# Kernel optimization log

Measured on AMD Instinct MI355X. Metric: run time of the kernel, lower is better.

Reference implementation:

```python
import jax, jax.numpy as jnp
import numpy as np


def setup_inputs() -> dict:
    key = jax.random.key(0)
    ks = jax.random.split(key, 8)
    B, S, H, E = 4, 4096, 768, 64
    hidden_states = jax.random.normal(ks[0], (B, S, H), dtype=jnp.float32)
    attention_mask = jnp.ones((B, S), dtype=jnp.float32)
    entity_positions = jax.random.randint(ks[1], (B, E), 0, S)
    scale = 1.0 / np.sqrt(H)
    Wq = jax.random.normal(ks[2], (H, H), dtype=jnp.float32) * scale
    bq = jnp.zeros((H,), dtype=jnp.float32)
    Wk = jax.random.normal(ks[3], (H, H), dtype=jnp.float32) * scale
    bk = jnp.zeros((H,), dtype=jnp.float32)
    Wv = jax.random.normal(ks[4], (H, H), dtype=jnp.float32) * scale
    bv = jnp.zeros((H,), dtype=jnp.float32)
    return {"hidden_states": hidden_states, "attention_mask": attention_mask,
            "entity_positions": entity_positions,
            "Wq": Wq, "bq": bq, "Wk": Wk, "bk": bk, "Wv": Wv, "bv": bv}


def reference(hidden_states, attention_mask, entity_positions, Wq, bq, Wk, bk, Wv, bv):
    B, S, H = hidden_states.shape
    scaling = jnp.sqrt(jnp.asarray(H, dtype=jnp.float32))
    # Linear layers (torch: x @ W.T + b)
    q = jnp.einsum('bsh,oh->bso', hidden_states, Wq) + bq
    k = jnp.einsum('bsh,oh->bso', hidden_states, Wk) + bk
    v = jnp.einsum('bsh,oh->bso', hidden_states, Wv) + bv
    scores = jnp.einsum('bqh,bkh->bqk', q, k) / scaling  # [B,S,S]
    # Entity bias: +1.0 added to every row at each entity column (duplicates accumulate).
    # Equivalent to a per-key-column bias broadcast over query rows.
    bias_cols = jnp.zeros((B, S), dtype=scores.dtype)
    batch_idx = jnp.arange(B)[:, None]  # [B,1] broadcast against [B,E]
    bias_cols = bias_cols.at[batch_idx, entity_positions].add(1.0)
    scores = scores + bias_cols[:, None, :]
    # Attention mask over key columns.
    scores = scores + (1.0 - attention_mask)[:, None, :] * -10000.0
    probs = jax.nn.softmax(scores, axis=-1)
    context = jnp.einsum('bqk,bkh->bqh', probs, v)
    return context
```

## Files before the change

### kernel.cpp

```cpp
#include <hip/hip_runtime.h>


typedef short bf16x8 __attribute__((ext_vector_type(8)));
typedef float f32x4 __attribute__((ext_vector_type(4)));
typedef float f32x16 __attribute__((ext_vector_type(16)));

#define MFMA16(a, b, c) __builtin_amdgcn_mfma_f32_16x16x32_bf16(a, b, c, 0, 0, 0)
#define MFMA32(a, b, c) __builtin_amdgcn_mfma_f32_32x32x16_bf16(a, b, c, 0, 0, 0)

#define ASM_BAR() asm volatile("s_barrier" ::: "memory")
#define ASM_WAITV0() asm volatile("s_waitcnt vmcnt(0)" ::: "memory")
#define ASM_WAITV4() asm volatile("s_waitcnt vmcnt(4)" ::: "memory")
#define ASM_WAITV6() asm volatile("s_waitcnt vmcnt(6)" ::: "memory")
#define ASM_WAITL0() asm volatile("s_waitcnt lgkmcnt(0)" ::: "memory")

__device__ __forceinline__ unsigned short f2bf(float f) {
  unsigned u = __float_as_uint(f);
  u = u + 0x7FFFu + ((u >> 16) & 1u);
  return (unsigned short)(u >> 16);
}

__device__ __forceinline__ void gll16(const void* g, void* l) {
  __builtin_amdgcn_global_load_lds(
      (const __attribute__((address_space(1))) unsigned int*)g,
      (__attribute__((address_space(3))) unsigned int*)l, 16, 0, 0);
}

#define SCALE_L2E 0.05205877316f
#define LOG2E 1.4426950408889634f

__global__ void convert_w_kernel(const float* __restrict__ w0, const float* __restrict__ w1,
                                 const float* __restrict__ w2, unsigned short* __restrict__ o0,
                                 unsigned short* __restrict__ o1, unsigned short* __restrict__ o2) {
  const int which = blockIdx.y;
  const float* s = which == 0 ? w0 : (which == 1 ? w1 : w2);
  unsigned short* d = which == 0 ? o0 : (which == 1 ? o1 : o2);
  const int i = (blockIdx.x * 256 + threadIdx.x) * 4;
  float4 v = *(const float4*)(s + i);
  ushort4 r = make_ushort4(f2bf(v.x), f2bf(v.y), f2bf(v.z), f2bf(v.w));
  *(ushort4*)(d + i) = r;
}

__global__ void convert_hs_kernel(const float* __restrict__ hs, unsigned short* __restrict__ o) {
  const int i = (blockIdx.x * 256 + threadIdx.x) * 4;
  float4 v = *(const float4*)(hs + i);
  ushort4 r = make_ushort4(f2bf(v.x), f2bf(v.y), f2bf(v.z), f2bf(v.w));
  *(ushort4*)(o + i) = r;
}

__global__ void kb_init_kernel(const float* __restrict__ mask, float* __restrict__ kb) {
  const int i = blockIdx.x * 256 + threadIdx.x;
  kb[i] = (1.0f - mask[i]) * (-10000.0f * LOG2E);
}

__global__ void kb_scatter_kernel(const int* __restrict__ ep, float* __restrict__ kb) {
  const int t = threadIdx.x;
  const int b = t >> 6, e = t & 63;
  const int pos = ep[b * 64 + e];
  atomicAdd(kb + b * 4096 + pos, LOG2E);
}

__global__ __launch_bounds__(256, 3) void gemm_qk_kernel(
    const unsigned short* __restrict__ hsb, const unsigned short* __restrict__ Wqb,
    const unsigned short* __restrict__ Wkb, const float* __restrict__ bq,
    const float* __restrict__ bk, unsigned short* __restrict__ Qb,
    unsigned short* __restrict__ Kb) {
  const int z = blockIdx.z;
  const unsigned short* W = z ? Wkb : Wqb;
  const float* bias = z ? bk : bq;
  unsigned short* out = z ? Kb : Qb;
  const int m0 = blockIdx.x * 128;
  const int n0 = blockIdx.y * 128;

  __shared__ __align__(16) unsigned short Ab[3][128 * 32];
  __shared__ __align__(16) unsigned short Bb[3][128 * 32];

  const int t = threadIdx.x;
  const int lane = t & 63;
  const int w = t >> 6;
  const int wm = w & 1, wn = w >> 1;

  f32x4 acc[4][4] = {};

  auto issueT = [&](const unsigned short* src, int base, int kk, unsigned short* dst) {
#pragma unroll
    for (int r = 0; r < 2; r++) {
      int u = r * 256 + t;
      int o = u >> 2, cc = u & 3;
      int c = cc ^ ((o >> 1) & 3);
      gll16(src + (size_t)(base + o) * 768 + kk + c * 8, dst + u * 8);
    }
  };

  issueT(hsb, m0, 0, Ab[0]);
  issueT(W, n0, 0, Bb[0]);
  issueT(hsb, m0, 32, Ab[1]);
  issueT(W, n0, 32, Bb[1]);
  ASM_WAITV4();
  ASM_BAR();

  for (int k = 0; k < 24; k++) {
    const int buf = k % 3;
    if (k < 22) {
      const int nb = (k + 2) % 3;
      issueT(hsb, m0, (k + 2) * 32, Ab[nb]);
      issueT(W, n0, (k + 2) * 32, Bb[nb]);
    }
    bf16x8 af[4], bfr[4];
#pragma unroll
    for (int mt = 0; mt < 4; mt++) {
      int row = wm * 64 + mt * 16 + (lane & 15);
      int cc = (lane >> 4) ^ ((row >> 1) & 3);
      af[mt] = *(const bf16x8*)(&Ab[buf][row * 32 + cc * 8]);
    }
#pragma unroll
    for (int nt = 0; nt < 4; nt++) {
      int row = wn * 64 + nt * 16 + (lane & 15);
      int cc = (lane >> 4) ^ ((row >> 1) & 3);
      bfr[nt] = *(const bf16x8*)(&Bb[buf][row * 32 + cc * 8]);
    }
#pragma unroll
    for (int mt = 0; mt < 4; mt++)
#pragma unroll
      for (int nt = 0; nt < 4; nt++) acc[mt][nt] = MFMA16(af[mt], bfr[nt], acc[mt][nt]);
    if (k < 22) {
      ASM_WAITV4();
    } else {
      ASM_WAITV0();
    }
    ASM_BAR();
  }

#pragma unroll
  for (int nt = 0; nt < 4; nt++) {
    int col = n0 + wn * 64 + nt * 16 + (lane & 15);
    float bv = bias[col];
#pragma unroll
    for (int mt = 0; mt < 4; mt++) {
#pragma unroll
      for (int i = 0; i < 4; i++) {
        int row = m0 + wm * 64 + mt * 16 + (lane >> 4) * 4 + i;
        out[(size_t)row * 768 + col] = f2bf(acc[mt][nt][i] + bv);
      }
    }
  }
}

__global__ __launch_bounds__(256, 3) void gemm_vt_kernel(const unsigned short* __restrict__ hsb,
                                                         const unsigned short* __restrict__ Wvb,
                                                         const float* __restrict__ bv,
                                                         unsigned short* __restrict__ Vt) {
  const int m0 = blockIdx.x * 128;
  const int n0 = blockIdx.y * 128;

  __shared__ __align__(16) unsigned short Ab[3][128 * 32];
  __shared__ __align__(16) unsigned short Bb[3][128 * 32];

  const int t = threadIdx.x;
  const int lane = t & 63;
  const int w = t >> 6;
  const int wm = w & 1, wn = w >> 1;

  f32x4 acc[4][4] = {};

  auto issueT = [&](const unsigned short* src, int base, int kk, unsigned short* dst) {
#pragma unroll
    for (int r = 0; r < 2; r++) {
      int u = r * 256 + t;
      int o = u >> 2, cc = u & 3;
      int c = cc ^ ((o >> 1) & 3);
      gll16(src + (size_t)(base + o) * 768 + kk + c * 8, dst + u * 8);
    }
  };

  issueT(Wvb, m0, 0, Ab[0]);
  issueT(hsb, n0, 0, Bb[0]);
  issueT(Wvb, m0, 32, Ab[1]);
  issueT(hsb, n0, 32, Bb[1]);
  ASM_WAITV4();
  ASM_BAR();

  for (int k = 0; k < 24; k++) {
    const int buf = k % 3;
    if (k < 22) {
      const int nb = (k + 2) % 3;
      issueT(Wvb, m0, (k + 2) * 32, Ab[nb]);
      issueT(hsb, n0, (k + 2) * 32, Bb[nb]);
    }
    bf16x8 af[4], bfr[4];
#pragma unroll
    for (int mt = 0; mt < 4; mt++) {
      int row = wm * 64 + mt * 16 + (lane & 15);
      int cc = (lane >> 4) ^ ((row >> 1) & 3);
      af[mt] = *(const bf16x8*)(&Ab[buf][row * 32 + cc * 8]);
    }
#pragma unroll
    for (int nt = 0; nt < 4; nt++) {
      int row = wn * 64 + nt * 16 + (lane & 15);
      int cc = (lane >> 4) ^ ((row >> 1) & 3);
      bfr[nt] = *(const bf16x8*)(&Bb[buf][row * 32 + cc * 8]);
    }
#pragma unroll
    for (int mt = 0; mt < 4; mt++)
#pragma unroll
      for (int nt = 0; nt < 4; nt++) acc[mt][nt] = MFMA16(af[mt], bfr[nt], acc[mt][nt]);
    if (k < 22) {
      ASM_WAITV4();
    } else {
      ASM_WAITV0();
    }
    ASM_BAR();
  }

#pragma unroll
  for (int mt = 0; mt < 4; mt++) {
#pragma unroll
    for (int i = 0; i < 4; i++) {
      int row_o = m0 + wm * 64 + mt * 16 + (lane >> 4) * 4 + i;
      float bb = bv[row_o];
#pragma unroll
      for (int nt = 0; nt < 4; nt++) {
        int mcol = n0 + wn * 64 + nt * 16 + (lane & 15);
        int bat = mcol >> 12, s = mcol & 4095;
        Vt[(size_t)bat * 768 * 4096 + (size_t)row_o * 4096 + s] = f2bf(acc[mt][nt][i] + bb);
      }
    }
  }
}

__global__ __launch_bounds__(512, 2) void flash_kernel(const unsigned short* __restrict__ Qb,
                                                       const unsigned short* __restrict__ Kb,
                                                       const unsigned short* __restrict__ Vt,
                                                       const float* __restrict__ KB,
                                                       float* __restrict__ out) {
  __shared__ __align__(16) unsigned short kbuf[32 * 768];
  __shared__ __align__(16) unsigned short vbuf[768 * 32];
  __shared__ __align__(16) unsigned short pbuf[4 * 64 * 8];
  __shared__ __align__(16) float sx[4 * 2 * 64 * 16];
  __shared__ __align__(16) float kb_lds[4096];
  __shared__ float st_l[64];

  const int t = threadIdx.x;
  const int lane = t & 63;
  const int w = t >> 6;
  const int rg = w & 1, hg = w >> 1;
  const int mt2 = w & 1, dg = w >> 1;
  const int flat = blockIdx.x;
  const int b = flat & 3, qt = flat >> 2;
  const int q0 = qt * 64;

  const unsigned short* Qg = Qb + (size_t)b * 4096 * 768;
  const unsigned short* Kg = Kb + (size_t)b * 4096 * 768;
  const unsigned short* Vg = Vt + (size_t)b * 768 * 4096;
  const float* KBb = KB + b * 4096;

  bf16x8 qf[12];
  {
    const unsigned short* qp =
        Qg + (size_t)(q0 + rg * 32 + (lane & 31)) * 768 + hg * 192 + (lane >> 5) * 8;
#pragma unroll
    for (int c = 0; c < 12; c++) qf[c] = *(const bf16x8*)(qp + c * 16);
  }
#pragma unroll
  for (int r = 0; r < 2; r++) {
    int i = t * 8 + r * 4;
    *(float4*)(kb_lds + i) = *(const float4*)(KBb + i);
  }

  int kidx[12];
  {
    const int key = lane & 31, l5 = lane >> 5, sw = (key >> 1) & 3;
#pragma unroll
    for (int c = 0; c < 12; c++) {
      int g = hg * 24 + c * 2 + l5;
      kidx[c] = ((g >> 2) * 128 + key * 4 + ((g & 3) ^ sw)) * 8;
    }
  }
  int vbase;
  {
    int d0 = dg * 192 + (lane & 15);
    vbase = (d0 * 4 + ((lane >> 4) ^ ((d0 >> 1) & 3))) * 8;
  }
  int pidx0, pidx1;
  {
    int g2 = lane >> 4;
    int r0 = mt2 * 32 + (lane & 15);
    pidx0 = (g2 * 64 + (r0 ^ (g2 * 2))) * 8;
    pidx1 = (g2 * 64 + ((r0 + 16) ^ (g2 * 2))) * 8;
  }
  const int s_rg = t >> 8, s_q = (t >> 6) & 3, s_l = t & 63;
  const int col = s_l & 31;
  const int row_b = s_rg * 32 + 8 * s_q + 4 * (s_l >> 5);
  int pslot[4];
#pragma unroll
  for (int jj = 0; jj < 4; jj++)
    pslot[jj] = ((col >> 3) * 64 + ((row_b + jj) ^ ((col >> 3) * 2))) * 8 + (col & 7);
  float* sxw = sx + hg * 2048 + (rg * 64 + lane) * 16;
  const int wswz = (lane >> 1) & 3;
  const float* sxr = sx + (s_rg * 64 + s_l) * 16 + (s_q ^ ((s_l >> 1) & 3)) * 4;

  f32x4 oacc[24] = {};
  float racc0 = 0.0f, racc1 = 0.0f, racc2 = 0.0f, racc3 = 0.0f;

  auto issueK = [&](int j) {
#pragma unroll
    for (int r = 0; r < 6; r++) {
      int u = r * 512 + t;
      int ks = u >> 7, rem = u & 127, key = rem >> 2, cs = rem & 3;
      int c = cs ^ ((key >> 1) & 3);
      gll16(Kg + (size_t)(j * 32 + key) * 768 + ks * 32 + c * 8, &kbuf[u * 8]);
    }
  };
  auto issueV = [&](int j) {
#pragma unroll
    for (int r = 0; r < 6; r++) {
      int u = r * 512 + t;
      int d = u >> 2, cs = u & 3;
      int c = cs ^ ((d >> 1) & 3);
      gll16(Vg + (size_t)d * 4096 + j * 32 + c * 8, &vbuf[u * 8]);
    }
  };

  issueK(0);
  ASM_WAITV0();
  ASM_BAR();

  for (int j = 0; j < 128; j++) {
    issueV(j);
    f32x16 s = {};
#pragma unroll
    for (int c = 0; c < 12; c++) {
      bf16x8 kf = *(const bf16x8*)(kbuf + kidx[c]);
      s = MFMA32(qf[c], kf, s);
    }
#pragma unroll
    for (int i = 0; i < 4; i++) {
      *(float4*)(sxw + (i ^ wswz) * 4) =
          make_float4(s[i * 4], s[i * 4 + 1], s[i * 4 + 2], s[i * 4 + 3]);
    }
    ASM_WAITL0();
    ASM_BAR();
    if (j < 127) issueK(j + 1);
    {
      float4 a0 = *(const float4*)(sxr);
      float4 a1 = *(const float4*)(sxr + 2048);
      float4 a2 = *(const float4*)(sxr + 4096);
      float4 a3 = *(const float4*)(sxr + 6144);
      float kbias = kb_lds[j * 32 + col];
      float e0 = __builtin_amdgcn_exp2f(fmaf(a0.x + a1.x + a2.x + a3.x, SCALE_L2E, kbias));
      float e1 = __builtin_amdgcn_exp2f(fmaf(a0.y + a1.y + a2.y + a3.y, SCALE_L2E, kbias));
      float e2 = __builtin_amdgcn_exp2f(fmaf(a0.z + a1.z + a2.z + a3.z, SCALE_L2E, kbias));
      float e3 = __builtin_amdgcn_exp2f(fmaf(a0.w + a1.w + a2.w + a3.w, SCALE_L2E, kbias));
      pbuf[pslot[0]] = f2bf(e0);
      pbuf[pslot[1]] = f2bf(e1);
      pbuf[pslot[2]] = f2bf(e2);
      pbuf[pslot[3]] = f2bf(e3);
      racc0 += e0;
      racc1 += e1;
      racc2 += e2;
      racc3 += e3;
    }
    ASM_WAITL0();
    if (j < 127) {
      ASM_WAITV6();
    } else {
      ASM_WAITV0();
    }
    ASM_BAR();
    {
      bf16x8 pf0 = *(const bf16x8*)(pbuf + pidx0);
      bf16x8 pf1 = *(const bf16x8*)(pbuf + pidx1);
#pragma unroll
      for (int dt = 0; dt < 12; dt++) {
        bf16x8 vf = *(const bf16x8*)(vbuf + vbase + dt * 512);
        oacc[dt] = MFMA16(pf0, vf, oacc[dt]);
        oacc[12 + dt] = MFMA16(pf1, vf, oacc[12 + dt]);
      }
    }
    ASM_WAITV0();
    ASM_BAR();
  }
#pragma unroll
  for (int m = 1; m < 32; m <<= 1) {
    racc0 += __shfl_xor(racc0, m, 32);
    racc1 += __shfl_xor(racc1, m, 32);
    racc2 += __shfl_xor(racc2, m, 32);
    racc3 += __shfl_xor(racc3, m, 32);
  }
  if ((s_l & 31) == 0) {
    st_l[row_b] = racc0;
    st_l[row_b + 1] = racc1;
    st_l[row_b + 2] = racc2;
    st_l[row_b + 3] = racc3;
  }
  __syncthreads();
#pragma unroll
  for (int pt = 0; pt < 2; pt++) {
    int rb = mt2 * 32 + pt * 16 + (lane >> 4) * 4;
    float l0 = 1.0f / st_l[rb], l1 = 1.0f / st_l[rb + 1];
    float l2 = 1.0f / st_l[rb + 2], l3 = 1.0f / st_l[rb + 3];
#pragma unroll
    for (int dt = 0; dt < 12; dt++) {
      int d = dg * 192 + dt * 16 + (lane & 15);
      size_t base = ((size_t)(b * 4096 + q0 + rb)) * 768 + d;
      out[base] = oacc[pt * 12 + dt][0] * l0;
      out[base + 768] = oacc[pt * 12 + dt][1] * l1;
      out[base + 2 * 768] = oacc[pt * 12 + dt][2] * l2;
      out[base + 3 * 768] = oacc[pt * 12 + dt][3] * l3;
    }
  }
}

extern "C" void kernel_launch(void* const* d_in, const int* in_sizes, int n_in, void* d_out,
                              int out_size, void* d_ws, size_t ws_size, hipStream_t stream) {
  const float* hs = (const float*)d_in[0];
  const float* mask = (const float*)d_in[1];
  const int* ep = (const int*)d_in[2];
  const float* Wq = (const float*)d_in[3];
  const float* bq = (const float*)d_in[4];
  const float* Wk = (const float*)d_in[5];
  const float* bk = (const float*)d_in[6];
  const float* Wv = (const float*)d_in[7];
  const float* bv = (const float*)d_in[8];
  float* outp = (float*)d_out;

  char* ws = (char*)d_ws;
  unsigned short* Qb = (unsigned short*)(ws);
  unsigned short* Kb = (unsigned short*)(ws + 25165824);
  unsigned short* Vt = (unsigned short*)(ws + 50331648);
  unsigned short* Wqb = (unsigned short*)(ws + 75497472);
  unsigned short* Wkb = (unsigned short*)(ws + 76677120);
  unsigned short* Wvb = (unsigned short*)(ws + 77856768);
  float* KBp = (float*)(ws + 79036416);
  unsigned short* Hsb = (unsigned short*)(ws + 79101952);

  convert_w_kernel<<<dim3(576, 3), 256, 0, stream>>>(Wq, Wk, Wv, Wqb, Wkb, Wvb);
  convert_hs_kernel<<<12288, 256, 0, stream>>>(hs, Hsb);
  kb_init_kernel<<<64, 256, 0, stream>>>(mask, KBp);
  kb_scatter_kernel<<<1, 256, 0, stream>>>(ep, KBp);
  gemm_qk_kernel<<<dim3(128, 6, 2), 256, 0, stream>>>(Hsb, Wqb, Wkb, bq, bk, Qb, Kb);
  gemm_vt_kernel<<<dim3(6, 128), 256, 0, stream>>>(Hsb, Wvb, bv, Vt);
  flash_kernel<<<256, 512, 0, stream>>>(Qb, Kb, Vt, KBp, outp);
}
```

Baseline: 484.0 us.

## Merge prep kernels and QKV GEMMs into single launches, tweak P LDS swizzle

Four small preprocessing kernels (weight/hidden-state bf16 conversion, key-bias init, entity scatter) are folded into one prep kernel, and the entity bias is now computed by per-column counting instead of atomics. The Q/K GEMM and the transposed V GEMM become one launch of 2304 blocks dispatched by block index. The flash kernel's P-buffer swizzle gains an extra XOR bit to reduce LDS bank conflicts. The aim is to cut launch overhead and tail gaps between kernels, at the cost of some branching and extra index arithmetic.

New measurement: 477.7 us, median of 2. No clear change (-1.3%).

```diff
diff --git a/kernel.cpp b/kernel.cpp
--- a/kernel.cpp
+++ b/kernel.cpp
@@ -29,56 +29,77 @@
 #define SCALE_L2E 0.05205877316f
 #define LOG2E 1.4426950408889634f
 
-__global__ void convert_w_kernel(const float* __restrict__ w0, const float* __restrict__ w1,
-                                 const float* __restrict__ w2, unsigned short* __restrict__ o0,
-                                 unsigned short* __restrict__ o1, unsigned short* __restrict__ o2) {
-  const int which = blockIdx.y;
-  const float* s = which == 0 ? w0 : (which == 1 ? w1 : w2);
-  unsigned short* d = which == 0 ? o0 : (which == 1 ? o1 : o2);
-  const int i = (blockIdx.x * 256 + threadIdx.x) * 4;
-  float4 v = *(const float4*)(s + i);
-  ushort4 r = make_ushort4(f2bf(v.x), f2bf(v.y), f2bf(v.z), f2bf(v.w));
-  *(ushort4*)(d + i) = r;
-}
-
-__global__ void convert_hs_kernel(const float* __restrict__ hs, unsigned short* __restrict__ o) {
-  const int i = (blockIdx.x * 256 + threadIdx.x) * 4;
-  float4 v = *(const float4*)(hs + i);
-  ushort4 r = make_ushort4(f2bf(v.x), f2bf(v.y), f2bf(v.z), f2bf(v.w));
-  *(ushort4*)(o + i) = r;
-}
-
-__global__ void kb_init_kernel(const float* __restrict__ mask, float* __restrict__ kb) {
-  const int i = blockIdx.x * 256 + threadIdx.x;
-  kb[i] = (1.0f - mask[i]) * (-10000.0f * LOG2E);
-}
-
-__global__ void kb_scatter_kernel(const int* __restrict__ ep, float* __restrict__ kb) {
+#define HS_BLOCKS 12288
+#define W_BLOCKS 1728
+#define KB_BLOCKS 64
+__global__ void prep_kernel(const float* __restrict__ hs, unsigned short* __restrict__ ohs,
+                            const float* __restrict__ w0, const float* __restrict__ w1,
+                            const float* __restrict__ w2, unsigned short* __restrict__ o0,
+                            unsigned short* __restrict__ o1, unsigned short* __restrict__ o2,
+                            const float* __restrict__ mask, const int* __restrict__ ep,
+                            float* __restrict__ kb) {
+  __shared__ int eps[64];
+  const int bid = blockIdx.x;
   const int t = threadIdx.x;
-  const int b = t >> 6, e = t & 63;
-  const int pos = ep[b * 64 + e];
-  atomicAdd(kb + b * 4096 + pos, LOG2E);
-}
-
-__global__ __launch_bounds__(256, 3) void gemm_qk_kernel(
+  if (bid < HS_BLOCKS) {
+    const int i = (bid * 256 + t) * 4;
+    float4 v = *(const float4*)(hs + i);
+    *(ushort4*)(ohs + i) = make_ushort4(f2bf(v.x), f2bf(v.y), f2bf(v.z), f2bf(v.w));
+  } else if (bid < HS_BLOCKS + W_BLOCKS) {
+    const int wb = bid - HS_BLOCKS;
+    const int which = wb / 576;
+    const float* s = which == 0 ? w0 : (which == 1 ? w1 : w2);
+    unsigned short* d = which == 0 ? o0 : (which == 1 ? o1 : o2);
+    const int i = ((wb - which * 576) * 256 + t) * 4;
+    float4 v = *(const float4*)(s + i);
+    *(ushort4*)(d + i) = make_ushort4(f2bf(v.x), f2bf(v.y), f2bf(v.z), f2bf(v.w));
+  } else {
+    const int s = (bid - HS_BLOCKS - W_BLOCKS) * 256 + t;
+    const int b = s >> 12;
+    if (t < 64) eps[t] = ep[b * 64 + t];
+    __syncthreads();
+    const int sp = s & 4095;
+    float cnt = 0.0f;
+#pragma unroll 8
+    for (int e = 0; e < 64; e++) cnt += (eps[e] == sp) ? 1.0f : 0.0f;
+    kb[s] = (1.0f - mask[s]) * (-10000.0f * LOG2E) + cnt * LOG2E;
+  }
+}
+
+__global__ __launch_bounds__(256, 3) void gemm_qkv_kernel(
     const unsigned short* __restrict__ hsb, const unsigned short* __restrict__ Wqb,
-    const unsigned short* __restrict__ Wkb, const float* __restrict__ bq,
-    const float* __restrict__ bk, unsigned short* __restrict__ Qb,
-    unsigned short* __restrict__ Kb) {
-  const int z = blockIdx.z;
-  const unsigned short* W = z ? Wkb : Wqb;
-  const float* bias = z ? bk : bq;
-  unsigned short* out = z ? Kb : Qb;
-  const int m0 = blockIdx.x * 128;
-  const int n0 = blockIdx.y * 128;
-
+    const unsigned short* __restrict__ Wkb, const unsigned short* __restrict__ Wvb,
+    const float* __restrict__ bq, const float* __restrict__ bk, const float* __restrict__ bv,
+    unsigned short* __restrict__ Qb, unsigned short* __restrict__ Kb,
+    unsigned short* __restrict__ Vt) {
   __shared__ __align__(16) unsigned short Ab[3][128 * 32];
   __shared__ __align__(16) unsigned short Bb[3][128 * 32];
 
+  const int bid = blockIdx.x;
   const int t = threadIdx.x;
   const int lane = t & 63;
   const int w = t >> 6;
   const int wm = w & 1, wn = w >> 1;
+
+  const bool is_vt = bid >= 1536;
+  const unsigned short* srcA;
+  const unsigned short* srcB;
+  int m0, n0, z = 0;
+  if (!is_vt) {
+    z = bid / 768;
+    const int r = bid - z * 768;
+    m0 = (r & 127) * 128;
+    n0 = (r >> 7) * 128;
+    srcA = hsb;
+    srcB = z ? Wkb : Wqb;
+  } else {
+    const int r = bid - 1536;
+    const int mx = r % 6;
+    m0 = mx * 128;
+    n0 = (r / 6) * 128;
+    srcA = Wvb;
+    srcB = hsb;
+  }
 
   f32x4 acc[4][4] = {};
 
@@ -92,10 +113,10 @@
     }
   };
 
-  issueT(hsb, m0, 0, Ab[0]);
-  issueT(W, n0, 0, Bb[0]);
-  issueT(hsb, m0, 32, Ab[1]);
-  issueT(W, n0, 32, Bb[1]);
+  issueT(srcA, m0, 0, Ab[0]);
+  issueT(srcB, n0, 0, Bb[0]);
+  issueT(srcA, m0, 32, Ab[1]);
+  issueT(srcB, n0, 32, Bb[1]);
   ASM_WAITV4();
   ASM_BAR();
 
@@ -103,8 +124,8 @@
     const int buf = k % 3;
     if (k < 22) {
       const int nb = (k + 2) % 3;
-      issueT(hsb, m0, (k + 2) * 32, Ab[nb]);
-      issueT(W, n0, (k + 2) * 32, Bb[nb]);
+      issueT(srcA, m0, (k + 2) * 32, Ab[nb]);
+      issueT(srcB, n0, (k + 2) * 32, Bb[nb]);
     }
     bf16x8 af[4], bfr[4];
 #pragma unroll
@@ -131,98 +152,35 @@
     ASM_BAR();
   }
 
-#pragma unroll
-  for (int nt = 0; nt < 4; nt++) {
-    int col = n0 + wn * 64 + nt * 16 + (lane & 15);
-    float bv = bias[col];
+  if (!is_vt) {
+    const float* bias = z ? bk : bq;
+    unsigned short* out = z ? Kb : Qb;
+#pragma unroll
+    for (int nt = 0; nt < 4; nt++) {
+      int col = n0 + wn * 64 + nt * 16 + (lane & 15);
+      float bv_ = bias[col];
+#pragma unroll
+      for (int mt = 0; mt < 4; mt++) {
+#pragma unroll
+        for (int i = 0; i < 4; i++) {
+          int row = m0 + wm * 64 + mt * 16 + (lane >> 4) * 4 + i;
+          out[(size_t)row * 768 + col] = f2bf(acc[mt][nt][i] + bv_);
+        }
+      }
+    }
+  } else {
 #pragma unroll
     for (int mt = 0; mt < 4; mt++) {
 #pragma unroll
       for (int i = 0; i < 4; i++) {
-        int row = m0 + wm * 64 + mt * 16 + (lane >> 4) * 4 + i;
-        out[(size_t)row * 768 + col] = f2bf(acc[mt][nt][i] + bv);
-      }
-    }
-  }
-}
-
-__global__ __launch_bounds__(256, 3) void gemm_vt_kernel(const unsigned short* __restrict__ hsb,
-                                                         const unsigned short* __restrict__ Wvb,
-                                                         const float* __restrict__ bv,
-                                                         unsigned short* __restrict__ Vt) {
-  const int m0 = blockIdx.x * 128;
-  const int n0 = blockIdx.y * 128;
-
-  __shared__ __align__(16) unsigned short Ab[3][128 * 32];
-  __shared__ __align__(16) unsigned short Bb[3][128 * 32];
-
-  const int t = threadIdx.x;
-  const int lane = t & 63;
-  const int w = t >> 6;
-  const int wm = w & 1, wn = w >> 1;
-
-  f32x4 acc[4][4] = {};
-
-  auto issueT = [&](const unsigned short* src, int base, int kk, unsigned short* dst) {
-#pragma unroll
-    for (int r = 0; r < 2; r++) {
-      int u = r * 256 + t;
-      int o = u >> 2, cc = u & 3;
-      int c = cc ^ ((o >> 1) & 3);
-      gll16(src + (size_t)(base + o) * 768 + kk + c * 8, dst + u * 8);
-    }
-  };
-
-  issueT(Wvb, m0, 0, Ab[0]);
-  issueT(hsb, n0, 0, Bb[0]);
-  issueT(Wvb, m0, 32, Ab[1]);
-  issueT(hsb, n0, 32, Bb[1]);
-  ASM_WAITV4();
-  ASM_BAR();
-
-  for (int k = 0; k < 24; k++) {
-    const int buf = k % 3;
-    if (k < 22) {
-      const int nb = (k + 2) % 3;
-      issueT(Wvb, m0, (k + 2) * 32, Ab[nb]);
-      issueT(hsb, n0, (k + 2) * 32, Bb[nb]);
-    }
-    bf16x8 af[4], bfr[4];
-#pragma unroll
-    for (int mt = 0; mt < 4; mt++) {
-      int row = wm * 64 + mt * 16 + (lane & 15);
-      int cc = (lane >> 4) ^ ((row >> 1) & 3);
-      af[mt] = *(const bf16x8*)(&Ab[buf][row * 32 + cc * 8]);
-    }
-#pragma unroll
-    for (int nt = 0; nt < 4; nt++) {
-      int row = wn * 64 + nt * 16 + (lane & 15);
-      int cc = (lane >> 4) ^ ((row >> 1) & 3);
-      bfr[nt] = *(const bf16x8*)(&Bb[buf][row * 32 + cc * 8]);
-    }
-#pragma unroll
-    for (int mt = 0; mt < 4; mt++)
-#pragma unroll
-      for (int nt = 0; nt < 4; nt++) acc[mt][nt] = MFMA16(af[mt], bfr[nt], acc[mt][nt]);
-    if (k < 22) {
-      ASM_WAITV4();
-    } else {
-      ASM_WAITV0();
-    }
-    ASM_BAR();
-  }
-
-#pragma unroll
-  for (int mt = 0; mt < 4; mt++) {
-#pragma unroll
-    for (int i = 0; i < 4; i++) {
-      int row_o = m0 + wm * 64 + mt * 16 + (lane >> 4) * 4 + i;
-      float bb = bv[row_o];
-#pragma unroll
-      for (int nt = 0; nt < 4; nt++) {
-        int mcol = n0 + wn * 64 + nt * 16 + (lane & 15);
-        int bat = mcol >> 12, s = mcol & 4095;
-        Vt[(size_t)bat * 768 * 4096 + (size_t)row_o * 4096 + s] = f2bf(acc[mt][nt][i] + bb);
+        int row_o = m0 + wm * 64 + mt * 16 + (lane >> 4) * 4 + i;
+        float bb = bv[row_o];
+#pragma unroll
+        for (int nt = 0; nt < 4; nt++) {
+          int mcol = n0 + wn * 64 + nt * 16 + (lane & 15);
+          int bat = mcol >> 12, s = mcol & 4095;
+          Vt[(size_t)bat * 768 * 4096 + (size_t)row_o * 4096 + s] = f2bf(acc[mt][nt][i] + bb);
+        }
       }
     }
   }
@@ -285,16 +243,19 @@
   {
     int g2 = lane >> 4;
     int r0 = mt2 * 32 + (lane & 15);
-    pidx0 = (g2 * 64 + (r0 ^ (g2 * 2))) * 8;
-    pidx1 = (g2 * 64 + ((r0 + 16) ^ (g2 * 2))) * 8;
+    int r1 = r0 + 16;
+    pidx0 = (g2 * 64 + (r0 ^ (g2 * 2) ^ ((r0 >> 2) & 1))) * 8;
+    pidx1 = (g2 * 64 + (r1 ^ (g2 * 2) ^ ((r1 >> 2) & 1))) * 8;
   }
   const int s_rg = t >> 8, s_q = (t >> 6) & 3, s_l = t & 63;
   const int col = s_l & 31;
   const int row_b = s_rg * 32 + 8 * s_q + 4 * (s_l >> 5);
   int pslot[4];
 #pragma unroll
-  for (int jj = 0; jj < 4; jj++)
-    pslot[jj] = ((col >> 3) * 64 + ((row_b + jj) ^ ((col >> 3) * 2))) * 8 + (col & 7);
+  for (int jj = 0; jj < 4; jj++) {
+    int rw = row_b + jj;
+    pslot[jj] = ((col >> 3) * 64 + (rw ^ ((col >> 3) * 2) ^ ((rw >> 2) & 1))) * 8 + (col & 7);
+  }
   float* sxw = sx + hg * 2048 + (rg * 64 + lane) * 16;
   const int wswz = (lane >> 1) & 3;
   const float* sxr = sx + (s_rg * 64 + s_l) * 16 + (s_q ^ ((s_l >> 1) & 3)) * 4;
@@ -434,11 +395,8 @@
   float* KBp = (float*)(ws + 79036416);
   unsigned short* Hsb = (unsigned short*)(ws + 79101952);
 
-  convert_w_kernel<<<dim3(576, 3), 256, 0, stream>>>(Wq, Wk, Wv, Wqb, Wkb, Wvb);
-  convert_hs_kernel<<<12288, 256, 0, stream>>>(hs, Hsb);
-  kb_init_kernel<<<64, 256, 0, stream>>>(mask, KBp);
-  kb_scatter_kernel<<<1, 256, 0, stream>>>(ep, KBp);
-  gemm_qk_kernel<<<dim3(128, 6, 2), 256, 0, stream>>>(Hsb, Wqb, Wkb, bq, bk, Qb, Kb);
-  gemm_vt_kernel<<<dim3(6, 128), 256, 0, stream>>>(Hsb, Wvb, bv, Vt);
+  prep_kernel<<<HS_BLOCKS + W_BLOCKS + KB_BLOCKS, 256, 0, stream>>>(
+      hs, Hsb, Wq, Wk, Wv, Wqb, Wkb, Wvb, mask, ep, KBp);
+  gemm_qkv_kernel<<<2304, 256, 0, stream>>>(Hsb, Wqb, Wkb, Wvb, bq, bk, bv, Qb, Kb, Vt);
   flash_kernel<<<256, 512, 0, stream>>>(Qb, Kb, Vt, KBp, outp);
 }
```
